# Kernel tuning notes

Hardware: AMD Instinct MI355X
Metric: run time of the kernel (lower is better)

The kernel has to match this reference:

```python
import jax, jax.numpy as jnp
import numpy as np
import math

N_QUBITS = 8
N_LAYERS = 3
BATCH = 8192
INPUT_DIM = 512


def _apply_1q(st, U, wire, batched):
    # st: (batch, 2,...,2) with N_QUBITS qubit axes; U: (2,2) or (batch,2,2)
    st = jnp.moveaxis(st, wire + 1, 1)
    sh = st.shape
    flat = st.reshape(sh[0], 2, -1)
    if batched:
        flat = jnp.einsum('bij,bjk->bik', U, flat)
    else:
        flat = jnp.einsum('ij,bjk->bik', U, flat)
    return jnp.moveaxis(flat.reshape(sh), 1, wire + 1)


def _apply_cnot(st, c, t):
    cax, tax = c + 1, t + 1
    zero = jnp.take(st, 0, axis=cax)
    one = jnp.take(st, 1, axis=cax)
    tax2 = tax - 1 if tax > cax else tax  # target axis shifts after control removed
    one = jnp.flip(one, axis=tax2)
    return jnp.stack([zero, one], axis=cax)


def _ry_batched(theta):
    # theta: (batch,) -> (batch,2,2) complex64
    c = jnp.cos(theta / 2)
    s = jnp.sin(theta / 2)
    row0 = jnp.stack([c, -s], axis=-1)
    row1 = jnp.stack([s, c], axis=-1)
    return jnp.stack([row0, row1], axis=-2).astype(jnp.complex64)


def _rot(phi, theta, omega):
    # PennyLane Rot = RZ(omega) RY(theta) RZ(phi), scalar params -> (2,2) complex64
    c = jnp.cos(theta / 2)
    s = jnp.sin(theta / 2)
    u00 = jnp.exp(-0.5j * (phi + omega)) * c
    u01 = -jnp.exp(0.5j * (phi - omega)) * s
    u10 = jnp.exp(-0.5j * (phi - omega)) * s
    u11 = jnp.exp(0.5j * (phi + omega)) * c
    return jnp.stack([jnp.stack([u00, u01]), jnp.stack([u10, u11])]).astype(jnp.complex64)


def _quantum_circuit(angles, q_weights):
    batch = angles.shape[0]
    st = jnp.zeros((batch, 2 ** N_QUBITS), jnp.complex64).at[:, 0].set(1.0)
    st = st.reshape((batch,) + (2,) * N_QUBITS)
    # AngleEmbedding with RY rotations
    for w in range(N_QUBITS):
        st = _apply_1q(st, _ry_batched(angles[:, w]), w, batched=True)
    # StronglyEntanglingLayers: Rot on each wire, then CNOT ring with range r
    for l in range(N_LAYERS):
        for w in range(N_QUBITS):
            st = _apply_1q(st, _rot(q_weights[l, w, 0], q_weights[l, w, 1], q_weights[l, w, 2]), w, batched=False)
        r = (l % (N_QUBITS - 1)) + 1
        for w in range(N_QUBITS):
            st = _apply_cnot(st, w, (w + r) % N_QUBITS)
    probs = st.real ** 2 + st.imag ** 2
    zs = []
    for w in range(N_QUBITS):
        p = jnp.moveaxis(probs, w + 1, 1).reshape(batch, 2, -1).sum(-1)
        zs.append(p[:, 0] - p[:, 1])  # <Z_w> = P(0) - P(1)
    return jnp.stack(zs, axis=-1)


def setup_inputs() -> dict:
    key = jax.random.key(0)
    k1, k2, k3 = jax.random.split(key, 3)
    x = jax.random.normal(k1, (BATCH, INPUT_DIM), dtype=jnp.float32)
    W = jax.random.normal(k2, (N_QUBITS, INPUT_DIM), dtype=jnp.float32) * (1.0 / math.sqrt(INPUT_DIM))
    b = jnp.zeros((N_QUBITS,), jnp.float32)
    scale = jnp.ones((N_QUBITS,), jnp.float32)
    bias = jnp.zeros((N_QUBITS,), jnp.float32)
    q_weights = 0.01 * jax.random.normal(k3, (N_LAYERS, N_QUBITS, 3), dtype=jnp.float32)
    return {"x": x, "W": W, "b": b, "scale": scale, "bias": bias, "q_weights": q_weights}


def reference(x, W, b, scale, bias, q_weights):
    proj = x @ W.T + b                                   # (batch, n_qubits)
    angles = jax.nn.sigmoid(proj * scale + bias) * jnp.float32(math.pi)
    return _quantum_circuit(angles, q_weights)           # (batch, n_qubits)
```

## Files before the change

### kernel.cpp

```cpp
#include <hip/hip_runtime.h>
#include <math.h>


namespace {

constexpr float PI_F = 3.14159265358979323846f;

struct Cx { float re, im; };

__device__ __forceinline__ float shfx(float v, int m) {
  return __shfl_xor(v, m, 64);
}

__device__ __forceinline__ void mix2(Cx &a, Cx &b,
    float u00r, float u00i, float u01r, float u01i,
    float u10r, float u10i, float u11r, float u11i) {
  float ar = a.re, ai = a.im, br = b.re, bi = b.im;
  a.re = u00r*ar - u00i*ai + u01r*br - u01i*bi;
  a.im = u00r*ai + u00i*ar + u01r*bi + u01i*br;
  b.re = u10r*ar - u10i*ai + u11r*br - u11i*bi;
  b.im = u10r*ai + u10i*ar + u11r*bi + u11i*br;
}

template<int W>
__device__ __forceinline__ void apply1q(Cx s[4],
    float u00r, float u00i, float u01r, float u01i,
    float u10r, float u10i, float u11r, float u11i, int lane) {
  if constexpr (W == 7) {
    mix2(s[0], s[1], u00r,u00i,u01r,u01i,u10r,u10i,u11r,u11i);
    mix2(s[2], s[3], u00r,u00i,u01r,u01i,u10r,u10i,u11r,u11i);
  } else if constexpr (W == 6) {
    mix2(s[0], s[2], u00r,u00i,u01r,u01i,u10r,u10i,u11r,u11i);
    mix2(s[1], s[3], u00r,u00i,u01r,u01i,u10r,u10i,u11r,u11i);
  } else {
    constexpr int lm = 1 << (5 - W);
    const bool hi = (lane & lm) != 0;
    float cAr = hi ? u11r : u00r, cAi = hi ? u11i : u00i;
    float cBr = hi ? u10r : u01r, cBi = hi ? u10i : u01i;
#pragma unroll
    for (int k = 0; k < 4; ++k) {
      float tr = shfx(s[k].re, lm), ti = shfx(s[k].im, lm);
      float mr = s[k].re, mi = s[k].im;
      s[k].re = cAr*mr - cAi*mi + cBr*tr - cBi*ti;
      s[k].im = cAr*mi + cAi*mr + cBr*ti + cBi*tr;
    }
  }
}

template<int W>
__device__ __forceinline__ void ryW(Cx s[4], float ang, int lane) {
  float h = 0.5f * ang;
  float c = __cosf(h), sn = __sinf(h);
  apply1q<W>(s, c, 0.f, -sn, 0.f, sn, 0.f, c, 0.f, lane);
}

template<int L, int W>
__device__ __forceinline__ void rotW(Cx s[4], const float* __restrict__ qw, int lane) {
  float phi = qw[L*24 + W*3 + 0];
  float th  = qw[L*24 + W*3 + 1];
  float om  = qw[L*24 + W*3 + 2];
  float c  = __cosf(0.5f*th), sn = __sinf(0.5f*th);
  float a  = 0.5f*(phi + om), d = 0.5f*(phi - om);
  float ca = __cosf(a), sa = __sinf(a);
  float cd = __cosf(d), sd = __sinf(d);
  apply1q<W>(s, c*ca, -c*sa, -sn*cd, -sn*sd, sn*cd, -sn*sd, c*ca, c*sa, lane);
}

__device__ __forceinline__ void swapc(Cx &a, Cx &b) { Cx t = a; a = b; b = t; }

__device__ __forceinline__ void cswap(Cx &a, Cx &b, bool c) {
  float ar = a.re, ai = a.im;
  a.re = c ? b.re : a.re;  a.im = c ? b.im : a.im;
  b.re = c ? ar : b.re;    b.im = c ? ai : b.im;
}

template<int CW, int TW>
__device__ __forceinline__ void cnot(Cx s[4], int lane) {
  constexpr int pc = 7 - CW, pt = 7 - TW;
  if constexpr (pc >= 2 && pt >= 2) {
    constexpr int lmC = 1 << (pc - 2), lmT = 1 << (pt - 2);
    const bool ctl = (lane & lmC) != 0;
#pragma unroll
    for (int k = 0; k < 4; ++k) {
      float tr = shfx(s[k].re, lmT), ti = shfx(s[k].im, lmT);
      s[k].re = ctl ? tr : s[k].re;
      s[k].im = ctl ? ti : s[k].im;
    }
  } else if constexpr (pc >= 2 && pt < 2) {
    constexpr int lmC = 1 << (pc - 2);
    const bool ctl = (lane & lmC) != 0;
    if constexpr (pt == 0) { cswap(s[0], s[1], ctl); cswap(s[2], s[3], ctl); }
    else                   { cswap(s[0], s[2], ctl); cswap(s[1], s[3], ctl); }
  } else if constexpr (pc < 2 && pt >= 2) {
    constexpr int lmT = 1 << (pt - 2);
    constexpr int k0 = (pc == 0) ? 1 : 2;
    s[k0].re = shfx(s[k0].re, lmT); s[k0].im = shfx(s[k0].im, lmT);
    s[3].re  = shfx(s[3].re,  lmT); s[3].im  = shfx(s[3].im,  lmT);
  } else {
    if constexpr (pc == 1) swapc(s[2], s[3]);
    else                   swapc(s[1], s[3]);
  }
}

template<int L>
__device__ __forceinline__ void rotLayer(Cx s[4], const float* __restrict__ qw, int lane) {
  rotW<L,0>(s, qw, lane); rotW<L,1>(s, qw, lane);
  rotW<L,2>(s, qw, lane); rotW<L,3>(s, qw, lane);
  rotW<L,4>(s, qw, lane); rotW<L,5>(s, qw, lane);
  rotW<L,6>(s, qw, lane); rotW<L,7>(s, qw, lane);
}

__global__ __launch_bounds__(256) void quantum_layer_kernel(
    const float* __restrict__ x, const float* __restrict__ Wm,
    const float* __restrict__ bvec, const float* __restrict__ scale,
    const float* __restrict__ bias, const float* __restrict__ qw,
    float* __restrict__ out) {
  const int tid  = threadIdx.x;
  const int lane = tid & 63;
  const int wv   = tid >> 6;
  const int b    = blockIdx.x * 4 + wv;

  const float4* x4 = (const float4*)(x + (size_t)b * 512);
  float4 xa = x4[lane];
  float4 xb = x4[64 + lane];
  float ang[8];
#pragma unroll
  for (int q = 0; q < 8; ++q) {
    const float4* w4 = (const float4*)(Wm + q * 512);
    float4 wa = w4[lane];
    float4 wb = w4[64 + lane];
    ang[q] = xa.x*wa.x + xa.y*wa.y + xa.z*wa.z + xa.w*wa.w
           + xb.x*wb.x + xb.y*wb.y + xb.z*wb.z + xb.w*wb.w;
  }
#pragma unroll
  for (int off = 32; off >= 1; off >>= 1)
#pragma unroll
    for (int q = 0; q < 8; ++q)
      ang[q] += shfx(ang[q], off);
#pragma unroll
  for (int q = 0; q < 8; ++q) {
    float t = (ang[q] + bvec[q]) * scale[q] + bias[q];
    ang[q] = PI_F / (1.f + __expf(-t));
  }

  Cx s[4];
#pragma unroll
  for (int k = 0; k < 4; ++k) { s[k].re = 0.f; s[k].im = 0.f; }
  s[0].re = (lane == 0) ? 1.f : 0.f;

  ryW<0>(s, ang[0], lane); ryW<1>(s, ang[1], lane);
  ryW<2>(s, ang[2], lane); ryW<3>(s, ang[3], lane);
  ryW<4>(s, ang[4], lane); ryW<5>(s, ang[5], lane);
  ryW<6>(s, ang[6], lane); ryW<7>(s, ang[7], lane);

  rotLayer<0>(s, qw, lane);
  cnot<0,1>(s, lane); cnot<1,2>(s, lane); cnot<2,3>(s, lane); cnot<3,4>(s, lane);
  cnot<4,5>(s, lane); cnot<5,6>(s, lane); cnot<6,7>(s, lane); cnot<7,0>(s, lane);

  rotLayer<1>(s, qw, lane);
  cnot<0,2>(s, lane); cnot<1,3>(s, lane); cnot<2,4>(s, lane); cnot<3,5>(s, lane);
  cnot<4,6>(s, lane); cnot<5,7>(s, lane); cnot<6,0>(s, lane); cnot<7,1>(s, lane);

  rotLayer<2>(s, qw, lane);
  cnot<0,3>(s, lane); cnot<1,4>(s, lane); cnot<2,5>(s, lane); cnot<3,6>(s, lane);
  cnot<4,7>(s, lane); cnot<5,0>(s, lane); cnot<6,1>(s, lane); cnot<7,2>(s, lane);

  float p0 = s[0].re*s[0].re + s[0].im*s[0].im;
  float p1 = s[1].re*s[1].re + s[1].im*s[1].im;
  float p2 = s[2].re*s[2].re + s[2].im*s[2].im;
  float p3 = s[3].re*s[3].re + s[3].im*s[3].im;
  float tot = p0 + p1 + p2 + p3;
  float z[8];
#pragma unroll
  for (int w = 0; w < 6; ++w)
    z[w] = ((lane >> (5 - w)) & 1) ? -tot : tot;
  z[6] = (p0 + p1) - (p2 + p3);
  z[7] = (p0 - p1) + (p2 - p3);
#pragma unroll
  for (int off = 32; off >= 1; off >>= 1)
#pragma unroll
    for (int w = 0; w < 8; ++w)
      z[w] += shfx(z[w], off);

  if (lane == 0) {
    float4* op = (float4*)(out + (size_t)b * 8);
    op[0] = make_float4(z[0], z[1], z[2], z[3]);
    op[1] = make_float4(z[4], z[5], z[6], z[7]);
  }
}

}

extern "C" void kernel_launch(void* const* d_in, const int* in_sizes, int n_in,
                              void* d_out, int out_size, void* d_ws, size_t ws_size,
                              hipStream_t stream) {
  const float* x     = (const float*)d_in[0];
  const float* Wm    = (const float*)d_in[1];
  const float* bvec  = (const float*)d_in[2];
  const float* scale = (const float*)d_in[3];
  const float* bias  = (const float*)d_in[4];
  const float* qw    = (const float*)d_in[5];
  float* out = (float*)d_out;

  constexpr int BATCH = 8192;
  constexpr int WAVES_PER_BLOCK = 4;
  dim3 grid(BATCH / WAVES_PER_BLOCK), block(WAVES_PER_BLOCK * 64);
  hipLaunchKernelGGL(quantum_layer_kernel, grid, block, 0, stream,
                     x, Wm, bvec, scale, bias, qw, out);
}
```

Before: 106.6 us.

## Map each batch sample to 16 lanes with 16 amplitudes per thread

Each sample's 256-amplitude state vector is now spread over 16 lanes holding 16 amplitudes each, instead of a full 64-lane wave holding 4 each. Gates on wires 4–7 become register-local operations, and only wires 0–3 need cross-lane shuffles. The projection dot product and the final reductions drop from 6 shuffle stages to 4. This cuts shuffle traffic and fits 4 samples per wave. In exchange, register pressure rises and occupancy may fall.

After: 100.2 us. -6.0%, faster.

```diff
diff --git a/kernel.cpp b/kernel.cpp
--- a/kernel.cpp
+++ b/kernel.cpp
@@ -23,22 +23,22 @@
 }
 
 template<int W>
-__device__ __forceinline__ void apply1q(Cx s[4],
+__device__ __forceinline__ void apply1q(Cx s[16],
     float u00r, float u00i, float u01r, float u01i,
     float u10r, float u10i, float u11r, float u11i, int lane) {
-  if constexpr (W == 7) {
-    mix2(s[0], s[1], u00r,u00i,u01r,u01i,u10r,u10i,u11r,u11i);
-    mix2(s[2], s[3], u00r,u00i,u01r,u01i,u10r,u10i,u11r,u11i);
-  } else if constexpr (W == 6) {
-    mix2(s[0], s[2], u00r,u00i,u01r,u01i,u10r,u10i,u11r,u11i);
-    mix2(s[1], s[3], u00r,u00i,u01r,u01i,u10r,u10i,u11r,u11i);
+  if constexpr (W >= 4) {
+    constexpr int step = 1 << (7 - W);
+#pragma unroll
+    for (int k = 0; k < 16; ++k)
+      if (!(k & step))
+        mix2(s[k], s[k + step], u00r,u00i,u01r,u01i,u10r,u10i,u11r,u11i);
   } else {
-    constexpr int lm = 1 << (5 - W);
+    constexpr int lm = 1 << (3 - W);
     const bool hi = (lane & lm) != 0;
     float cAr = hi ? u11r : u00r, cAi = hi ? u11i : u00i;
     float cBr = hi ? u10r : u01r, cBi = hi ? u10i : u01i;
 #pragma unroll
-    for (int k = 0; k < 4; ++k) {
+    for (int k = 0; k < 16; ++k) {
       float tr = shfx(s[k].re, lm), ti = shfx(s[k].im, lm);
       float mr = s[k].re, mi = s[k].im;
       s[k].re = cAr*mr - cAi*mi + cBr*tr - cBi*ti;
@@ -48,14 +48,14 @@
 }
 
 template<int W>
-__device__ __forceinline__ void ryW(Cx s[4], float ang, int lane) {
+__device__ __forceinline__ void ryW(Cx s[16], float ang, int lane) {
   float h = 0.5f * ang;
   float c = __cosf(h), sn = __sinf(h);
   apply1q<W>(s, c, 0.f, -sn, 0.f, sn, 0.f, c, 0.f, lane);
 }
 
 template<int L, int W>
-__device__ __forceinline__ void rotW(Cx s[4], const float* __restrict__ qw, int lane) {
+__device__ __forceinline__ void rotW(Cx s[16], const float* __restrict__ qw, int lane) {
   float phi = qw[L*24 + W*3 + 0];
   float th  = qw[L*24 + W*3 + 1];
   float om  = qw[L*24 + W*3 + 2];
@@ -75,35 +75,41 @@
 }
 
 template<int CW, int TW>
-__device__ __forceinline__ void cnot(Cx s[4], int lane) {
+__device__ __forceinline__ void cnot(Cx s[16], int lane) {
   constexpr int pc = 7 - CW, pt = 7 - TW;
-  if constexpr (pc >= 2 && pt >= 2) {
-    constexpr int lmC = 1 << (pc - 2), lmT = 1 << (pt - 2);
+  if constexpr (pc >= 4 && pt >= 4) {
+    constexpr int lmC = 1 << (pc - 4), lmT = 1 << (pt - 4);
     const bool ctl = (lane & lmC) != 0;
 #pragma unroll
-    for (int k = 0; k < 4; ++k) {
+    for (int k = 0; k < 16; ++k) {
       float tr = shfx(s[k].re, lmT), ti = shfx(s[k].im, lmT);
       s[k].re = ctl ? tr : s[k].re;
       s[k].im = ctl ? ti : s[k].im;
     }
-  } else if constexpr (pc >= 2 && pt < 2) {
-    constexpr int lmC = 1 << (pc - 2);
+  } else if constexpr (pc >= 4) {
+    constexpr int lmC = 1 << (pc - 4), step = 1 << pt;
     const bool ctl = (lane & lmC) != 0;
-    if constexpr (pt == 0) { cswap(s[0], s[1], ctl); cswap(s[2], s[3], ctl); }
-    else                   { cswap(s[0], s[2], ctl); cswap(s[1], s[3], ctl); }
-  } else if constexpr (pc < 2 && pt >= 2) {
-    constexpr int lmT = 1 << (pt - 2);
-    constexpr int k0 = (pc == 0) ? 1 : 2;
-    s[k0].re = shfx(s[k0].re, lmT); s[k0].im = shfx(s[k0].im, lmT);
-    s[3].re  = shfx(s[3].re,  lmT); s[3].im  = shfx(s[3].im,  lmT);
+#pragma unroll
+    for (int k = 0; k < 16; ++k)
+      if (!(k & step)) cswap(s[k], s[k + step], ctl);
+  } else if constexpr (pt >= 4) {
+    constexpr int lmT = 1 << (pt - 4), cb = 1 << pc;
+#pragma unroll
+    for (int k = 0; k < 16; ++k)
+      if (k & cb) {
+        s[k].re = shfx(s[k].re, lmT);
+        s[k].im = shfx(s[k].im, lmT);
+      }
   } else {
-    if constexpr (pc == 1) swapc(s[2], s[3]);
-    else                   swapc(s[1], s[3]);
+    constexpr int cb = 1 << pc, tb = 1 << pt;
+#pragma unroll
+    for (int k = 0; k < 16; ++k)
+      if ((k & cb) && !(k & tb)) swapc(s[k], s[k + tb]);
   }
 }
 
 template<int L>
-__device__ __forceinline__ void rotLayer(Cx s[4], const float* __restrict__ qw, int lane) {
+__device__ __forceinline__ void rotLayer(Cx s[16], const float* __restrict__ qw, int lane) {
   rotW<L,0>(s, qw, lane); rotW<L,1>(s, qw, lane);
   rotW<L,2>(s, qw, lane); rotW<L,3>(s, qw, lane);
   rotW<L,4>(s, qw, lane); rotW<L,5>(s, qw, lane);
@@ -117,23 +123,27 @@
     float* __restrict__ out) {
   const int tid  = threadIdx.x;
   const int lane = tid & 63;
-  const int wv   = tid >> 6;
-  const int b    = blockIdx.x * 4 + wv;
+  const int ll   = lane & 15;
+  const int b    = blockIdx.x * 16 + (tid >> 4);
 
   const float4* x4 = (const float4*)(x + (size_t)b * 512);
-  float4 xa = x4[lane];
-  float4 xb = x4[64 + lane];
+  float4 xs[8];
+#pragma unroll
+  for (int j = 0; j < 8; ++j) xs[j] = x4[j * 16 + ll];
+  const float4* W4 = (const float4*)Wm;
   float ang[8];
 #pragma unroll
   for (int q = 0; q < 8; ++q) {
-    const float4* w4 = (const float4*)(Wm + q * 512);
-    float4 wa = w4[lane];
-    float4 wb = w4[64 + lane];
-    ang[q] = xa.x*wa.x + xa.y*wa.y + xa.z*wa.z + xa.w*wa.w
-           + xb.x*wb.x + xb.y*wb.y + xb.z*wb.z + xb.w*wb.w;
-  }
-#pragma unroll
-  for (int off = 32; off >= 1; off >>= 1)
+    float acc = 0.f;
+#pragma unroll
+    for (int j = 0; j < 8; ++j) {
+      float4 w = W4[q * 128 + j * 16 + ll];
+      acc += xs[j].x*w.x + xs[j].y*w.y + xs[j].z*w.z + xs[j].w*w.w;
+    }
+    ang[q] = acc;
+  }
+#pragma unroll
+  for (int off = 8; off >= 1; off >>= 1)
 #pragma unroll
     for (int q = 0; q < 8; ++q)
       ang[q] += shfx(ang[q], off);
@@ -143,10 +153,10 @@
     ang[q] = PI_F / (1.f + __expf(-t));
   }
 
-  Cx s[4];
-#pragma unroll
-  for (int k = 0; k < 4; ++k) { s[k].re = 0.f; s[k].im = 0.f; }
-  s[0].re = (lane == 0) ? 1.f : 0.f;
+  Cx s[16];
+#pragma unroll
+  for (int k = 0; k < 16; ++k) { s[k].re = 0.f; s[k].im = 0.f; }
+  s[0].re = (ll == 0) ? 1.f : 0.f;
 
   ryW<0>(s, ang[0], lane); ryW<1>(s, ang[1], lane);
   ryW<2>(s, ang[2], lane); ryW<3>(s, ang[3], lane);
@@ -165,24 +175,40 @@
   cnot<0,3>(s, lane); cnot<1,4>(s, lane); cnot<2,5>(s, lane); cnot<3,6>(s, lane);
   cnot<4,7>(s, lane); cnot<5,0>(s, lane); cnot<6,1>(s, lane); cnot<7,2>(s, lane);
 
-  float p0 = s[0].re*s[0].re + s[0].im*s[0].im;
-  float p1 = s[1].re*s[1].re + s[1].im*s[1].im;
-  float p2 = s[2].re*s[2].re + s[2].im*s[2].im;
-  float p3 = s[3].re*s[3].re + s[3].im*s[3].im;
-  float tot = p0 + p1 + p2 + p3;
+  float p[16];
+#pragma unroll
+  for (int k = 0; k < 16; ++k) p[k] = s[k].re*s[k].re + s[k].im*s[k].im;
+
+  float q0[8], z7 = 0.f;
+#pragma unroll
+  for (int m = 0; m < 8; ++m) {
+    q0[m] = p[2*m] + p[2*m+1];
+    z7 += p[2*m] - p[2*m+1];
+  }
+  float q1[4], z6 = 0.f;
+#pragma unroll
+  for (int m = 0; m < 4; ++m) {
+    q1[m] = q0[2*m] + q0[2*m+1];
+    z6 += q0[2*m] - q0[2*m+1];
+  }
+  float q2a = q1[0] + q1[1], q2b = q1[2] + q1[3];
+  float z5  = (q1[0] - q1[1]) + (q1[2] - q1[3]);
+  float tot = q2a + q2b;
+  float z4  = q2a - q2b;
+
   float z[8];
 #pragma unroll
-  for (int w = 0; w < 6; ++w)
-    z[w] = ((lane >> (5 - w)) & 1) ? -tot : tot;
-  z[6] = (p0 + p1) - (p2 + p3);
-  z[7] = (p0 - p1) + (p2 - p3);
-#pragma unroll
-  for (int off = 32; off >= 1; off >>= 1)
+  for (int w = 0; w < 4; ++w)
+    z[w] = ((ll >> (3 - w)) & 1) ? -tot : tot;
+  z[4] = z4; z[5] = z5; z[6] = z6; z[7] = z7;
+
+#pragma unroll
+  for (int off = 8; off >= 1; off >>= 1)
 #pragma unroll
     for (int w = 0; w < 8; ++w)
       z[w] += shfx(z[w], off);
 
-  if (lane == 0) {
+  if (ll == 0) {
     float4* op = (float4*)(out + (size_t)b * 8);
     op[0] = make_float4(z[0], z[1], z[2], z[3]);
     op[1] = make_float4(z[4], z[5], z[6], z[7]);
@@ -203,8 +229,7 @@
   float* out = (float*)d_out;
 
   constexpr int BATCH = 8192;
-  constexpr int WAVES_PER_BLOCK = 4;
-  dim3 grid(BATCH / WAVES_PER_BLOCK), block(WAVES_PER_BLOCK * 64);
+  dim3 grid(BATCH / 16), block(256);
   hipLaunchKernelGGL(quantum_layer_kernel, grid, block, 0, stream,
                      x, Wm, bvec, scale, bias, qw, out);
 }
```

## Precompute circuit unitary and apply it as a bf16 MFMA GEMM

Applied to the files above, without the earlier changes.

Splits the work into two kernels. The first builds the 256x256 unitary of the fixed parameterized layers by simulating each basis column and stores it in bf16 in the workspace. The second computes the product-state embedding amplitudes per sample, multiplies them by the unitary with MFMA bf16 instructions, and reduces the resulting probabilities to Z expectations. This replaces the per-sample gate-by-gate shuffle simulation with dense tensor-core matrix work. The cost is bf16 rounding of both the state and the unitary, plus an extra kernel launch.

After: 105.3 us (median of 2 runs). No clear change (-1.2%).

```diff
diff --git a/kernel.cpp b/kernel.cpp
--- a/kernel.cpp
+++ b/kernel.cpp
@@ -6,11 +6,23 @@
 
 constexpr float PI_F = 3.14159265358979323846f;
 
+typedef short     bf16x8  __attribute__((ext_vector_type(8)));
+typedef float     f32x4   __attribute__((ext_vector_type(4)));
+typedef unsigned short u16x8 __attribute__((ext_vector_type(8)));
+typedef unsigned short u16x4 __attribute__((ext_vector_type(4)));
+
 struct Cx { float re, im; };
 
 __device__ __forceinline__ float shfx(float v, int m) {
   return __shfl_xor(v, m, 64);
 }
+
+__device__ __forceinline__ unsigned short f2bf(float f) {
+  unsigned u = __builtin_bit_cast(unsigned, f);
+  unsigned r = u + 0x7fff + ((u >> 16) & 1);
+  return (unsigned short)(r >> 16);
+}
+
 
 __device__ __forceinline__ void mix2(Cx &a, Cx &b,
     float u00r, float u00i, float u01r, float u01i,
@@ -47,13 +59,6 @@
   }
 }
 
-template<int W>
-__device__ __forceinline__ void ryW(Cx s[4], float ang, int lane) {
-  float h = 0.5f * ang;
-  float c = __cosf(h), sn = __sinf(h);
-  apply1q<W>(s, c, 0.f, -sn, 0.f, sn, 0.f, c, 0.f, lane);
-}
-
 template<int L, int W>
 __device__ __forceinline__ void rotW(Cx s[4], const float* __restrict__ qw, int lane) {
   float phi = qw[L*24 + W*3 + 0];
@@ -110,82 +115,206 @@
   rotW<L,6>(s, qw, lane); rotW<L,7>(s, qw, lane);
 }
 
-__global__ __launch_bounds__(256) void quantum_layer_kernel(
-    const float* __restrict__ x, const float* __restrict__ Wm,
-    const float* __restrict__ bvec, const float* __restrict__ scale,
-    const float* __restrict__ bias, const float* __restrict__ qw,
-    float* __restrict__ out) {
+__global__ __launch_bounds__(256) void build_u_kernel(
+    const float* __restrict__ qw, unsigned short* __restrict__ Bt) {
+  __shared__ __align__(16) float ucol[4 * 512];
   const int tid  = threadIdx.x;
   const int lane = tid & 63;
   const int wv   = tid >> 6;
-  const int b    = blockIdx.x * 4 + wv;
-
-  const float4* x4 = (const float4*)(x + (size_t)b * 512);
-  float4 xa = x4[lane];
-  float4 xb = x4[64 + lane];
-  float ang[8];
-#pragma unroll
-  for (int q = 0; q < 8; ++q) {
-    const float4* w4 = (const float4*)(Wm + q * 512);
-    float4 wa = w4[lane];
-    float4 wb = w4[64 + lane];
-    ang[q] = xa.x*wa.x + xa.y*wa.y + xa.z*wa.z + xa.w*wa.w
-           + xb.x*wb.x + xb.y*wb.y + xb.z*wb.z + xb.w*wb.w;
-  }
-#pragma unroll
-  for (int off = 32; off >= 1; off >>= 1)
-#pragma unroll
-    for (int q = 0; q < 8; ++q)
-      ang[q] += shfx(ang[q], off);
-#pragma unroll
-  for (int q = 0; q < 8; ++q) {
-    float t = (ang[q] + bvec[q]) * scale[q] + bias[q];
-    ang[q] = PI_F / (1.f + __expf(-t));
-  }
+  const int j    = blockIdx.x * 4 + wv;
 
   Cx s[4];
 #pragma unroll
   for (int k = 0; k < 4; ++k) { s[k].re = 0.f; s[k].im = 0.f; }
-  s[0].re = (lane == 0) ? 1.f : 0.f;
-
-  ryW<0>(s, ang[0], lane); ryW<1>(s, ang[1], lane);
-  ryW<2>(s, ang[2], lane); ryW<3>(s, ang[3], lane);
-  ryW<4>(s, ang[4], lane); ryW<5>(s, ang[5], lane);
-  ryW<6>(s, ang[6], lane); ryW<7>(s, ang[7], lane);
+  const int jl = j >> 2, jk = j & 3;
+#pragma unroll
+  for (int k = 0; k < 4; ++k)
+    s[k].re = (lane == jl && k == jk) ? 1.f : 0.f;
 
   rotLayer<0>(s, qw, lane);
   cnot<0,1>(s, lane); cnot<1,2>(s, lane); cnot<2,3>(s, lane); cnot<3,4>(s, lane);
   cnot<4,5>(s, lane); cnot<5,6>(s, lane); cnot<6,7>(s, lane); cnot<7,0>(s, lane);
-
   rotLayer<1>(s, qw, lane);
   cnot<0,2>(s, lane); cnot<1,3>(s, lane); cnot<2,4>(s, lane); cnot<3,5>(s, lane);
   cnot<4,6>(s, lane); cnot<5,7>(s, lane); cnot<6,0>(s, lane); cnot<7,1>(s, lane);
-
   rotLayer<2>(s, qw, lane);
   cnot<0,3>(s, lane); cnot<1,4>(s, lane); cnot<2,5>(s, lane); cnot<3,6>(s, lane);
   cnot<4,7>(s, lane); cnot<5,0>(s, lane); cnot<6,1>(s, lane); cnot<7,2>(s, lane);
 
-  float p0 = s[0].re*s[0].re + s[0].im*s[0].im;
-  float p1 = s[1].re*s[1].re + s[1].im*s[1].im;
-  float p2 = s[2].re*s[2].re + s[2].im*s[2].im;
-  float p3 = s[3].re*s[3].re + s[3].im*s[3].im;
-  float tot = p0 + p1 + p2 + p3;
-  float z[8];
-#pragma unroll
-  for (int w = 0; w < 6; ++w)
-    z[w] = ((lane >> (5 - w)) & 1) ? -tot : tot;
-  z[6] = (p0 + p1) - (p2 + p3);
-  z[7] = (p0 - p1) + (p2 - p3);
-#pragma unroll
-  for (int off = 32; off >= 1; off >>= 1)
-#pragma unroll
-    for (int w = 0; w < 8; ++w)
-      z[w] += shfx(z[w], off);
-
-  if (lane == 0) {
-    float4* op = (float4*)(out + (size_t)b * 8);
-    op[0] = make_float4(z[0], z[1], z[2], z[3]);
-    op[1] = make_float4(z[4], z[5], z[6], z[7]);
+  float* dst = &ucol[wv*512 + lane*8];
+  dst[0]=s[0].re; dst[1]=s[0].im; dst[2]=s[1].re; dst[3]=s[1].im;
+  dst[4]=s[2].re; dst[5]=s[2].im; dst[6]=s[3].re; dst[7]=s[3].im;
+  __syncthreads();
+
+  const int j0 = blockIdx.x * 4;
+#pragma unroll
+  for (int rep = 0; rep < 2; ++rep) {
+    int n = tid + rep * 256;
+    u16x4 v;
+#pragma unroll
+    for (int jj = 0; jj < 4; ++jj) v[jj] = f2bf(ucol[jj*512 + n]);
+    *(u16x4*)(Bt + (size_t)n * 256 + j0) = v;
+  }
+}
+
+
+__global__ __launch_bounds__(256) void qgemm_kernel(
+    const float* __restrict__ x, const float* __restrict__ Wm,
+    const float* __restrict__ bvec, const float* __restrict__ scale,
+    const float* __restrict__ bias, const unsigned short* __restrict__ Bt,
+    float* __restrict__ out) {
+  constexpr int APITCH = 264;
+  __shared__ __align__(16) unsigned short Ash[32 * APITCH];
+  __shared__ __align__(16) float tTab[32][16];
+  __shared__ __align__(16) float zpart[4][32][8];
+
+  const int tid  = threadIdx.x;
+  const int lane = tid & 63;
+  const int wv   = tid >> 6;
+  const int b0   = blockIdx.x * 32;
+
+  {
+    const int row = tid >> 3, oct = tid & 7;
+    const float4* xr = (const float4*)(x + (size_t)(b0 + row) * 512) + oct * 16;
+    float4 xs[16];
+#pragma unroll
+    for (int jj = 0; jj < 16; ++jj) xs[jj] = xr[jj];
+    float acc[8];
+#pragma unroll
+    for (int q = 0; q < 8; ++q) {
+      const float4* wr = (const float4*)(Wm + q * 512) + oct * 16;
+      float a = 0.f;
+#pragma unroll
+      for (int jj = 0; jj < 16; ++jj) {
+        float4 w = wr[jj];
+        a += xs[jj].x*w.x + xs[jj].y*w.y + xs[jj].z*w.z + xs[jj].w*w.w;
+      }
+      acc[q] = a;
+    }
+#pragma unroll
+    for (int off = 1; off <= 4; off <<= 1)
+#pragma unroll
+      for (int q = 0; q < 8; ++q)
+        acc[q] += shfx(acc[q], off);
+    if (oct == 0) {
+#pragma unroll
+      for (int q = 0; q < 8; ++q) {
+        float t = (acc[q] + bvec[q]) * scale[q] + bias[q];
+        float ang = PI_F / (1.f + __expf(-t));
+        float h = 0.5f * ang;
+        tTab[row][q]     = __cosf(h);
+        tTab[row][8 + q] = __sinf(h);
+      }
+    }
+  }
+  __syncthreads();
+
+  {
+    const int row = tid >> 3, oct = tid & 7;
+    float T[8][2];
+#pragma unroll
+    for (int w = 0; w < 8; ++w) { T[w][0] = tTab[row][w]; T[w][1] = tTab[row][8+w]; }
+    float H = T[0][(oct >> 2) & 1] * T[1][(oct >> 1) & 1] * T[2][oct & 1];
+    float a1[2], a2[4], a3[8], a4[16], a5[32];
+    a1[0] = H * T[3][0]; a1[1] = H * T[3][1];
+#pragma unroll
+    for (int u = 0; u < 2; ++u) { a2[u*2] = a1[u]*T[4][0]; a2[u*2+1] = a1[u]*T[4][1]; }
+#pragma unroll
+    for (int u = 0; u < 4; ++u) { a3[u*2] = a2[u]*T[5][0]; a3[u*2+1] = a2[u]*T[5][1]; }
+#pragma unroll
+    for (int u = 0; u < 8; ++u) { a4[u*2] = a3[u]*T[6][0]; a4[u*2+1] = a3[u]*T[6][1]; }
+#pragma unroll
+    for (int u = 0; u < 16; ++u){ a5[u*2] = a4[u]*T[7][0]; a5[u*2+1] = a4[u]*T[7][1]; }
+    unsigned short* arow = &Ash[row * APITCH + oct * 32];
+#pragma unroll
+    for (int g = 0; g < 4; ++g) {
+      u16x8 v;
+#pragma unroll
+      for (int e = 0; e < 8; ++e) v[e] = f2bf(a5[g*8 + e]);
+      *(u16x8*)(arow + g * 8) = v;
+    }
+  }
+  __syncthreads();
+
+  const int ln = lane & 15, quad = lane >> 4;
+  f32x4 acc[2][8];
+#pragma unroll
+  for (int mt = 0; mt < 2; ++mt)
+#pragma unroll
+    for (int nt = 0; nt < 8; ++nt) acc[mt][nt] = (f32x4){0.f, 0.f, 0.f, 0.f};
+
+#pragma unroll
+  for (int ks = 0; ks < 8; ++ks) {
+    const int k0 = ks * 32 + quad * 8;
+    bf16x8 af[2], bf[8];
+#pragma unroll
+    for (int mt = 0; mt < 2; ++mt)
+      af[mt] = *(const bf16x8*)(&Ash[(mt*16 + ln) * APITCH + k0]);
+#pragma unroll
+    for (int nt = 0; nt < 8; ++nt)
+      bf[nt] = *(const bf16x8*)(Bt + (size_t)(wv*128 + nt*16 + ln) * 256 + k0);
+#pragma unroll
+    for (int mt = 0; mt < 2; ++mt)
+#pragma unroll
+      for (int nt = 0; nt < 8; ++nt)
+        acc[mt][nt] = __builtin_amdgcn_mfma_f32_16x16x32_bf16(
+            af[mt], bf[nt], acc[mt][nt], 0, 0, 0);
+  }
+
+#pragma unroll
+  for (int mt = 0; mt < 2; ++mt)
+#pragma unroll
+    for (int r = 0; r < 4; ++r) {
+      float p[8];
+#pragma unroll
+      for (int nt = 0; nt < 8; ++nt) {
+        float v = acc[mt][nt][r];
+        float v2 = v * v;
+        p[nt] = v2 + shfx(v2, 1);
+      }
+      float u0[4], S4 = 0.f;
+#pragma unroll
+      for (int m2 = 0; m2 < 4; ++m2) {
+        u0[m2] = p[2*m2] + p[2*m2+1];
+        S4 += p[2*m2] - p[2*m2+1];
+      }
+      float u1[2], S3 = 0.f;
+#pragma unroll
+      for (int m2 = 0; m2 < 2; ++m2) {
+        u1[m2] = u0[2*m2] + u0[2*m2+1];
+        S3 += u0[2*m2] - u0[2*m2+1];
+      }
+      float S  = u1[0] + u1[1];
+      float S2 = u1[0] - u1[1];
+      float s5 = (lane & 8) ? -S : S;
+      float s6 = (lane & 4) ? -S : S;
+      float s7 = (lane & 2) ? -S : S;
+      float Tt = S;
+#pragma unroll
+      for (int off = 2; off <= 8; off <<= 1) {
+        Tt += shfx(Tt, off); s5 += shfx(s5, off); s6 += shfx(s6, off);
+        s7 += shfx(s7, off); S2 += shfx(S2, off); S3 += shfx(S3, off);
+        S4 += shfx(S4, off);
+      }
+      if (ln == 0) {
+        const int m = mt*16 + quad*4 + r;
+        float z0 = (wv & 2) ? -Tt : Tt;
+        float z1 = (wv & 1) ? -Tt : Tt;
+        *(float4*)&zpart[wv][m][0] = make_float4(z0, z1, S2, S3);
+        *(float4*)&zpart[wv][m][4] = make_float4(S4, s5, s6, s7);
+      }
+    }
+  __syncthreads();
+
+  if (tid < 64) {
+    const int m = tid >> 1, h = tid & 1;
+    float4 a = *(float4*)&zpart[0][m][h*4];
+    float4 b = *(float4*)&zpart[1][m][h*4];
+    float4 c = *(float4*)&zpart[2][m][h*4];
+    float4 d = *(float4*)&zpart[3][m][h*4];
+    float4 rsl = make_float4(a.x+b.x+c.x+d.x, a.y+b.y+c.y+d.y,
+                             a.z+b.z+c.z+d.z, a.w+b.w+c.w+d.w);
+    *(float4*)(out + (size_t)(b0 + m) * 8 + h * 4) = rsl;
   }
 }
 
@@ -201,10 +330,11 @@
   const float* bias  = (const float*)d_in[4];
   const float* qw    = (const float*)d_in[5];
   float* out = (float*)d_out;
-
-  constexpr int BATCH = 8192;
-  constexpr int WAVES_PER_BLOCK = 4;
-  dim3 grid(BATCH / WAVES_PER_BLOCK), block(WAVES_PER_BLOCK * 64);
-  hipLaunchKernelGGL(quantum_layer_kernel, grid, block, 0, stream,
-                     x, Wm, bvec, scale, bias, qw, out);
-}
+  (void)in_sizes; (void)n_in; (void)out_size; (void)ws_size;
+
+  unsigned short* Bt = (unsigned short*)d_ws;
+
+  hipLaunchKernelGGL(build_u_kernel, dim3(64), dim3(256), 0, stream, qw, Bt);
+  hipLaunchKernelGGL(qgemm_kernel, dim3(256), dim3(256), 0, stream,
+                     x, Wm, bvec, scale, bias, Bt, out);
+}
```
